# Kernel optimization log

Hardware: AMD Instinct MI355X
Metric: run time of the kernel (lower is better)

The kernel has to match this reference:

```python
import jax, jax.numpy as jnp
import numpy as np
import math

B, C, W, H = 4, 64, 128, 128
S = 2                 # len(shifts)
SHIFTS = (1, 2)       # dilations
HC = C // S           # hidden_channels = 32
NL = 8                # num_layer (8 diff stencils)
AREA = W * H
EPS = 1e-5


def _base_kernels():
    # 4 forward diff stencils + their 180-degree flips (delta2 = delta1[:, :, ::-1, ::-1])
    d1 = np.array([[[-1, 0, 0], [0, 1, 0], [0, 0, 0]],
                   [[0, -1, 0], [0, 1, 0], [0, 0, 0]],
                   [[0, 0, -1], [0, 1, 0], [0, 0, 0]],
                   [[0, 0, 0], [0, 1, -1], [0, 0, 0]]], dtype=np.float32).reshape(4, 1, 3, 3)
    d2 = d1[:, :, ::-1, ::-1].copy()
    return np.concatenate([d1, d2], axis=0)  # (8, 1, 3, 3)

# Depthwise kernel: per input channel, all 8 stencils (feature_group_count=HC layout)
_DW_KERNEL = jnp.asarray(np.tile(_base_kernels()[None], (HC, 1, 1, 1, 1)).reshape(NL * HC, 1, 3, 3))


def setup_inputs() -> dict:
    key = jax.random.key(0)
    ks = jax.random.split(key, 6)
    s = 0.05
    return {
        "x": jax.random.normal(ks[0], (B, C, W, H), jnp.float32),
        "trans_w": jax.random.normal(ks[1], (C, C), jnp.float32) * s,
        "bn1_g": jnp.ones((C,), jnp.float32),
        "bn1_b": jnp.zeros((C,), jnp.float32),
        "query_w": jax.random.normal(ks[2], (S, HC, HC), jnp.float32) * s,
        "key_w": jax.random.normal(ks[3], (S, (NL + 1) * HC, (NL + 1) * HC), jnp.float32) * s,
        "out_w": jax.random.normal(ks[4], (C, C), jnp.float32) * s,
        "bn2_g": jnp.ones((C,), jnp.float32),
        "bn2_b": jnp.zeros((C,), jnp.float32),
    }


def _bn_relu(y, g, b):
    # train-mode BatchNorm2d (biased batch stats) + ReLU
    m = y.mean((0, 2, 3), keepdims=True)
    v = y.var((0, 2, 3), keepdims=True)
    return jax.nn.relu((y - m) * jax.lax.rsqrt(v + EPS) * g[None, :, None, None] + b[None, :, None, None])


def _dw_diff_convs(x, dil):
    # x: (B, HC, W, H) -> 8 depthwise dilated 3x3 diff convs, concat order kernel-major
    y = jax.lax.conv_general_dilated(
        x, _DW_KERNEL, window_strides=(1, 1), padding='SAME',
        rhs_dilation=(dil, dil), feature_group_count=HC,
        dimension_numbers=('NCHW', 'OIHW', 'NCHW'))
    # grouped layout is (channel, stencil); torch concat order is (stencil, channel)
    return y.reshape(B, HC, NL, W, H).transpose(0, 2, 1, 3, 4).reshape(B, NL * HC, W, H)


def _inorm(w):
    # InstanceNorm2d(affine=False) over the last two dims, per (batch, shift)
    m = w.mean((-2, -1), keepdims=True)
    v = w.var((-2, -1), keepdims=True)
    return (w - m) * jax.lax.rsqrt(v + EPS)


def _l2n(x):
    # F.normalize(dim=-1)
    n = jnp.linalg.norm(x, axis=-1, keepdims=True)
    return x / jnp.maximum(n, 1e-12)


def reference(x, trans_w, bn1_g, bn1_b, query_w, key_w, out_w, bn2_g, bn2_b):
    y = _bn_relu(jnp.einsum('bchw,oc->bohw', x, trans_w), bn1_g, bn1_b)
    cens = y.reshape(B, S, HC, W, H)  # torch.chunk along channels
    keys, qrys, svs = [], [], []
    for i in range(S):
        c = cens[:, i]
        sur = _dw_diff_convs(c, SHIFTS[i])                                      # (B, 8*HC, W, H)
        kk = jnp.einsum('bchw,oc->bohw', jnp.concatenate([sur, c], 1), key_w[i])
        qq = jnp.einsum('bchw,oc->bohw', c, query_w[i])
        keys.append(kk.reshape(B, (NL + 1) * HC, AREA))
        qrys.append(qq.reshape(B, HC, AREA))
        svs.append(sur.reshape(B, NL * HC, AREA))
    keys = _l2n(jnp.stack(keys, 1))     # (B, S, 9*HC, AREA)
    qrys = _l2n(jnp.stack(qrys, 1))     # (B, S, HC, AREA)
    svs = jnp.stack(svs, 1)             # (B, S, 8*HC, AREA)
    w = jnp.einsum('bsca,bska->bsck', qrys, keys) / math.sqrt(AREA)  # (B, S, HC, 9*HC)
    sw = jax.nn.softmax(_inorm(w[..., :NL * HC]), axis=-1)           # (B, S, HC, 8*HC)
    out = jnp.einsum('bsck,bska->bsca', sw, svs).reshape(B, C, W, H)
    return _bn_relu(jnp.einsum('bchw,oc->bohw', out, out_w), bn2_g, bn2_b)
```

## Files before the change

kernel.cpp:

```cpp
#include <hip/hip_runtime.h>

#define BB 4
#define CC 64
#define SS 2
#define HCC 32
#define AREA_ 16384
#define KDIM 288
#define YPITCH 44

typedef _Float16 half8 __attribute__((ext_vector_type(8)));
typedef float f32x16 __attribute__((ext_vector_type(16)));

static __device__ __forceinline__ float warp_rsum(float v){
#pragma unroll
  for (int o=32;o>0;o>>=1) v += __shfl_down(v,o,64);
  return v;
}
static __device__ __forceinline__ float warp_rmax(float v){
#pragma unroll
  for (int o=32;o>0;o>>=1) v = fmaxf(v,__shfl_down(v,o,64));
  return v;
}

__global__ __launch_bounds__(256) void conv64_kernel(const float* __restrict__ in,
    const float* __restrict__ wmat, float* __restrict__ out){
  int b = blockIdx.x >> 7;
  int p0 = (blockIdx.x & 127) << 7;
  __shared__ float tile[64][132];
  __shared__ float wsm[64][68];
  for (int idx = threadIdx.x; idx < 4096; idx += 256){
    int c = idx & 63, o = idx >> 6;
    wsm[c][o] = wmat[o*64 + c];
  }
  const float* inb = in + (size_t)b*CC*AREA_ + p0;
  for (int idx = threadIdx.x; idx < 8192; idx += 256){
    int c = idx >> 7, pp = idx & 127;
    tile[c][pp] = inb[(size_t)c*AREA_ + pp];
  }
  __syncthreads();
  int px = (threadIdx.x & 31) * 4;
  int og = threadIdx.x >> 5;
  float4 acc[8];
#pragma unroll
  for (int i=0;i<8;i++) acc[i] = make_float4(0.f,0.f,0.f,0.f);
  for (int c=0;c<64;c++){
    float4 v  = *(const float4*)&tile[c][px];
    float4 w0 = *(const float4*)&wsm[c][og*8];
    float4 w1 = *(const float4*)&wsm[c][og*8+4];
    float wv[8] = {w0.x,w0.y,w0.z,w0.w,w1.x,w1.y,w1.z,w1.w};
#pragma unroll
    for (int i=0;i<8;i++){
      acc[i].x = fmaf(wv[i], v.x, acc[i].x);
      acc[i].y = fmaf(wv[i], v.y, acc[i].y);
      acc[i].z = fmaf(wv[i], v.z, acc[i].z);
      acc[i].w = fmaf(wv[i], v.w, acc[i].w);
    }
  }
  float* ob = out + (size_t)b*CC*AREA_ + p0 + px;
#pragma unroll
  for (int i=0;i<8;i++)
    *(float4*)&ob[(size_t)(og*8+i)*AREA_] = acc[i];
}

__global__ __launch_bounds__(256) void bn_part_kernel(const float* __restrict__ src,
    float* __restrict__ part){
  int c = blockIdx.x, chunk = blockIdx.y;
  float s1=0.f, s2=0.f;
  for (int b=0;b<BB;b++){
    const float* p = src + ((size_t)b*CC + c)*AREA_ + chunk*2048;
    for (int i=threadIdx.x;i<2048;i+=256){ float v=p[i]; s1+=v; s2+=v*v; }
  }
  __shared__ float red[8];
  float w1 = warp_rsum(s1), w2 = warp_rsum(s2);
  int lane = threadIdx.x & 63, wid = threadIdx.x >> 6;
  if (lane==0){ red[wid]=w1; red[4+wid]=w2; }
  __syncthreads();
  if (threadIdx.x==0){
    atomicAdd(&part[c], red[0]+red[1]+red[2]+red[3]);
    atomicAdd(&part[64+c], red[4]+red[5]+red[6]+red[7]);
  }
}

__global__ void bn_fin_kernel(const float* __restrict__ part, const float* __restrict__ gam,
    const float* __restrict__ bet, float* __restrict__ sb){
  int c = threadIdx.x;
  const float N = (float)(BB*AREA_);
  float m = part[c]/N;
  float var = part[64+c]/N - m*m;
  float sc = gam[c]*rsqrtf(var + 1e-5f);
  sb[c] = sc;
  sb[64+c] = bet[c] - m*sc;
}

__global__ __launch_bounds__(256) void bn_apply_relu_kernel(const float* __restrict__ src,
    const float* __restrict__ sb, float* __restrict__ dst){
  size_t i = (size_t)blockIdx.x*256 + threadIdx.x;
  int c = (int)((i >> 14) & 63);
  float v = fmaf(src[i], sb[c], sb[64+c]);
  dst[i] = v > 0.f ? v : 0.f;
}

__global__ __launch_bounds__(256) void qq_kernel(const float* __restrict__ y,
    const float* __restrict__ qw, float* __restrict__ qq){
  int blk = blockIdx.x;
  int p0 = (blk & 127) << 7;
  int s = (blk >> 7) & 1;
  int b = blk >> 8;
  __shared__ float tile[32][132];
  __shared__ float wsm[32][36];
  const float* qws = qw + s*HCC*HCC;
  for (int idx=threadIdx.x; idx<1024; idx+=256){
    int c = idx & 31, o = idx >> 5;
    wsm[c][o] = qws[o*32 + c];
  }
  const float* yb = y + ((size_t)b*CC + s*HCC)*AREA_ + p0;
  for (int idx=threadIdx.x; idx<4096; idx+=256){
    int c=idx>>7, pp=idx&127;
    tile[c][pp] = yb[(size_t)c*AREA_ + pp];
  }
  __syncthreads();
  int px = (threadIdx.x & 31) * 4;
  int og = threadIdx.x >> 5;
  float4 acc[4];
#pragma unroll
  for (int i=0;i<4;i++) acc[i] = make_float4(0.f,0.f,0.f,0.f);
  for (int c=0;c<32;c++){
    float4 v  = *(const float4*)&tile[c][px];
    float4 w0 = *(const float4*)&wsm[c][og*4];
    float wv[4] = {w0.x,w0.y,w0.z,w0.w};
#pragma unroll
    for (int i=0;i<4;i++){
      acc[i].x = fmaf(wv[i], v.x, acc[i].x);
      acc[i].y = fmaf(wv[i], v.y, acc[i].y);
      acc[i].z = fmaf(wv[i], v.z, acc[i].z);
      acc[i].w = fmaf(wv[i], v.w, acc[i].w);
    }
  }
  float* ob = qq + ((size_t)(b*SS+s)*HCC)*AREA_ + p0 + px;
#pragma unroll
  for (int i=0;i<4;i++)
    *(float4*)&ob[(size_t)(og*4+i)*AREA_] = acc[i];
}

__global__ __launch_bounds__(256,2) void gram_kernel(const float* __restrict__ y,
    const float* __restrict__ qq, float* __restrict__ dpart, float* __restrict__ wpart){
  const int PAarr[6]={0,0,1,0,1,2}, PBarr[6]={0,1,1,2,2,2};
  const int pairOrder[6]={1,3,4,0,2,5};
  const int pairbase[6]={0,262144,524288,786432,917504,1048576};
  const int tsz[6]={16384,16384,16384,8192,8192,4096};
  int bid = blockIdx.x;
  int bs = bid & 7;
  int sidx = bid >> 3;
  int pair = pairOrder[sidx >> 4];
  int slotIdx = sidx & 15;
  int Kstart = slotIdx << 10;
  const int nch = 16;
  int PA = PAarr[pair], PB = PBarr[pair];
  int RA = PA<2?128:64, CB = PB<2?128:64;
  bool diag = (PA==PB);
  int rows_tot = RA + (diag?0:CB);
  int passes = rows_tot >> 5;
  int s = bs & 1, b = bs >> 1, dil = 1+s;
  const float* yb = y + ((size_t)b*CC + s*HCC)*AREA_;
  const float* qqb = qq + (size_t)bs*HCC*AREA_;
  __shared__ __align__(16) _Float16 Us[256*64];
  int tid = threadIdx.x;
  int hq = tid & 7, rr8 = tid >> 3;
  int lane = tid & 63, wid = tid >> 6;
  int rbase = (wid>>1)*64, cbase = (wid&1)*64;
  bool active = (rbase < RA) && (cbase < CB);
  int boff = diag ? 0 : RA;
  int r0 = rbase + (lane&31), r1 = r0+32;
  int cr0 = boff + cbase + (lane&31), cr1 = cr0+32;
  int uo = lane>>5;

  auto loadPass = [&](int t, int p)->half8{
    int k0 = Kstart + t*64;
    int w = k0>>7, h = (k0&127) + hq*8;
    int pr = p*32 + rr8;
    int pan, prow;
    if (pr < RA){ pan = PA; prow = pr; } else { pan = PB; prow = pr - RA; }
    float vv[8];
    if (pan < 2){
      int l = pan*4 + (prow>>5), ch = prow & 31;
      int oy = ((0x6A40 >> (2*l)) & 3) - 1;
      int ox = ((0x6A4  >> (2*l)) & 3) - 1;
      const float* crow = yb + (size_t)ch*AREA_ + w*128 + h;
      float4 ca = *(const float4*)crow;
      float4 cb = *(const float4*)(crow+4);
      float cen[8] = {ca.x,ca.y,ca.z,ca.w,cb.x,cb.y,cb.z,cb.w};
      float nb[8];
      int wy = w + oy*dil, oxd = ox*dil, hb = h + oxd;
      if (wy>=0 && wy<128){
        const float* nrow = yb + (size_t)ch*AREA_ + wy*128 + hb;
        if (hb>=0 && hb<=120){
          float4 na, nc;
          __builtin_memcpy(&na, nrow, 16);
          __builtin_memcpy(&nc, nrow+4, 16);
          nb[0]=na.x; nb[1]=na.y; nb[2]=na.z; nb[3]=na.w;
          nb[4]=nc.x; nb[5]=nc.y; nb[6]=nc.z; nb[7]=nc.w;
        } else {
#pragma unroll
          for (int j=0;j<8;j++){
            int hx = hb + j;
            nb[j] = (hx>=0 && hx<128) ? nrow[j] : 0.f;
          }
        }
      } else {
#pragma unroll
        for (int j=0;j<8;j++) nb[j]=0.f;
      }
#pragma unroll
      for (int j=0;j<8;j++) vv[j] = cen[j]-nb[j];
    } else {
      const float* src = (prow<32) ? yb + (size_t)prow*AREA_ : qqb + (size_t)(prow-32)*AREA_;
      const float* crow = src + w*128 + h;
      float4 ca = *(const float4*)crow;
      float4 cb = *(const float4*)(crow+4);
      vv[0]=ca.x; vv[1]=ca.y; vv[2]=ca.z; vv[3]=ca.w;
      vv[4]=cb.x; vv[5]=cb.y; vv[6]=cb.z; vv[7]=cb.w;
    }
    half8 hv;
#pragma unroll
    for (int j=0;j<8;j++) hv[j] = (_Float16)vv[j];
    return hv;
  };
  auto writeLDS = [&](int p, half8 hv){
    int pr = p*32 + rr8;
    *(half8*)&Us[(size_t)pr*64 + ((hq ^ (pr&7))<<3)] = hv;
  };

  bool p4 = (passes >= 4), p6 = (passes >= 6), p8 = (passes >= 8);
  half8 f0{}, f1{}, f2{}, f3{}, f4{}, f5{}, f6{}, f7{};

  f32x16 acc00={}, acc01={}, acc10={}, acc11={};
  f0 = loadPass(0,0); f1 = loadPass(0,1);
  if (p4){ f2 = loadPass(0,2); f3 = loadPass(0,3); }
  if (p6){ f4 = loadPass(0,4); f5 = loadPass(0,5); }
  if (p8){ f6 = loadPass(0,6); f7 = loadPass(0,7); }
  for (int t=0; t<nch; ++t){
    asm volatile("s_waitcnt lgkmcnt(0)" ::: "memory");
    __builtin_amdgcn_s_barrier();
    writeLDS(0,f0); writeLDS(1,f1);
    if (p4){ writeLDS(2,f2); writeLDS(3,f3); }
    if (p6){ writeLDS(4,f4); writeLDS(5,f5); }
    if (p8){ writeLDS(6,f6); writeLDS(7,f7); }
    if (t+1 < nch){
      f0 = loadPass(t+1,0); f1 = loadPass(t+1,1);
      if (p4){ f2 = loadPass(t+1,2); f3 = loadPass(t+1,3); }
      if (p6){ f4 = loadPass(t+1,4); f5 = loadPass(t+1,5); }
      if (p8){ f6 = loadPass(t+1,6); f7 = loadPass(t+1,7); }
    }
    asm volatile("s_waitcnt lgkmcnt(0)" ::: "memory");
    __builtin_amdgcn_s_barrier();
    if (active){
#pragma unroll
      for (int st=0; st<4; ++st){
        int u = st*2 + uo;
        half8 a0 = *(const half8*)&Us[(size_t)r0*64  + ((u^(r0&7))<<3)];
        half8 a1 = *(const half8*)&Us[(size_t)r1*64  + ((u^(r1&7))<<3)];
        half8 b0 = *(const half8*)&Us[(size_t)cr0*64 + ((u^(cr0&7))<<3)];
        half8 b1 = *(const half8*)&Us[(size_t)cr1*64 + ((u^(cr1&7))<<3)];
        acc00 = __builtin_amdgcn_mfma_f32_32x32x16_f16(a0,b0,acc00,0,0,0);
        acc01 = __builtin_amdgcn_mfma_f32_32x32x16_f16(a0,b1,acc01,0,0,0);
        acc10 = __builtin_amdgcn_mfma_f32_32x32x16_f16(a1,b0,acc10,0,0,0);
        acc11 = __builtin_amdgcn_mfma_f32_32x32x16_f16(a1,b1,acc11,0,0,0);
      }
    }
  }
  if (active){
    size_t off = (size_t)bs*1114112 + pairbase[pair] + (size_t)slotIdx*tsz[pair];
    float* pp = (off < 4194304) ? (dpart + off) : (wpart + (off - 4194304));
    int cp = (pair<3)?128:64;
    int rr = 4*uo, cc = lane&31;
#pragma unroll
    for (int reg=0;reg<16;reg++){
      int ro = (reg&3) + 8*(reg>>2) + rr;
      pp[(size_t)(rbase+ro)*cp + cbase+cc]       = acc00[reg];
      pp[(size_t)(rbase+ro)*cp + cbase+32+cc]    = acc01[reg];
      pp[(size_t)(rbase+32+ro)*cp + cbase+cc]    = acc10[reg];
      pp[(size_t)(rbase+32+ro)*cp + cbase+32+cc] = acc11[reg];
    }
  }
}

__global__ __launch_bounds__(256) void reduce_kernel(const float* __restrict__ dpart,
    const float* __restrict__ wpart, float* __restrict__ P){
  const int PAarr[6]={0,0,1,0,1,2}, PBarr[6]={0,1,1,2,2,2};
  const int pairbase[6]={0,262144,524288,786432,917504,1048576};
  const int tsz[6]={16384,16384,16384,8192,8192,4096};
  const int chunkbase[7]={0,16,32,48,56,64,68};
  int chunk = blockIdx.x, bs = blockIdx.y;
  int pair = 0;
  while (chunk >= chunkbase[pair+1]) pair++;
  int lc = chunk - chunkbase[pair];
  int CN = (pair<3)?128:64;
  int Roff = PAarr[pair]*128, Coff = PBarr[pair]*128;
  int csh = (CN==128)?7:6;
  int cell0 = lc*1024 + threadIdx.x*4;
  int r = cell0 >> csh, c = cell0 & (CN-1);
  float4 v = make_float4(0.f,0.f,0.f,0.f);
  size_t base = (size_t)bs*1114112 + pairbase[pair];
  for (int k=0;k<16;k++){
    size_t off = base + (size_t)k*tsz[pair];
    const float* pp = (off < 4194304) ? (dpart + off) : (wpart + (off - 4194304));
    float4 t = *(const float4*)&pp[(size_t)r*CN + c];
    v.x += t.x; v.y += t.y; v.z += t.z; v.w += t.w;
  }
  float* Pb = P + (size_t)bs*102400;
  *(float4*)&Pb[(size_t)(Roff+r)*320 + Coff+c] = v;
  Pb[(size_t)(Coff+c  )*320 + Roff+r] = v.x;
  Pb[(size_t)(Coff+c+1)*320 + Roff+r] = v.y;
  Pb[(size_t)(Coff+c+2)*320 + Roff+r] = v.z;
  Pb[(size_t)(Coff+c+3)*320 + Roff+r] = v.w;
}

__global__ __launch_bounds__(256) void kwT_kernel(const float* __restrict__ kw, float* __restrict__ kwT){
  int idx = blockIdx.x*256 + threadIdx.x;
  if (idx >= 2*KDIM*KDIM) return;
  int s = idx / (KDIM*KDIM);
  int r = idx - s*KDIM*KDIM;
  int k = r / KDIM, j = r - k*KDIM;
  kwT[(size_t)s*KDIM*KDIM + (size_t)j*KDIM + k] = kw[idx];
}

__global__ __launch_bounds__(256) void vknorm_kernel(const float* __restrict__ P,
    const float* __restrict__ kwT, float* __restrict__ kn){
  int j = blockIdx.x, bs = blockIdx.y;
  int s = bs & 1;
  __shared__ float prow[KDIM];
  const float* Pb = P + (size_t)bs*102400 + (size_t)j*320;
  for (int i=threadIdx.x;i<KDIM;i+=256) prow[i]=Pb[i];
  __syncthreads();
  const float* kt = kwT + (size_t)s*KDIM*KDIM;
  int k = threadIdx.x;
  float acc=0.f;
  for (int jp=0;jp<KDIM;jp++) acc = fmaf(prow[jp], kt[(size_t)jp*KDIM + k], acc);
  atomicAdd(&kn[bs*256 + k], kt[(size_t)j*KDIM + k] * acc);
}

__global__ __launch_bounds__(256) void wmat_kernel(const float* __restrict__ P,
    const float* __restrict__ kwT, const float* __restrict__ kn,
    float* __restrict__ wbuf, float* __restrict__ wstats){
  int bs = blockIdx.x >> 5, c = blockIdx.x & 31;
  int s = bs & 1;
  __shared__ float prow[KDIM];
  const float* PbB = P + (size_t)bs*102400;
  const float* Pb = PbB + (size_t)(288+c)*320;
  for (int i=threadIdx.x;i<KDIM;i+=256) prow[i]=Pb[i];
  __syncthreads();
  const float* kt = kwT + (size_t)s*KDIM*KDIM;
  int k = threadIdx.x;
  float acc=0.f;
  for (int j=0;j<KDIM;j++) acc = fmaf(prow[j], kt[(size_t)j*KDIM + k], acc);
  float rk = 1.f/fmaxf(sqrtf(fmaxf(kn[bs*256+k],0.f)),1e-12f);
  float qn = PbB[(size_t)(288+c)*320 + 288+c];
  float rq = 1.f/fmaxf(sqrtf(fmaxf(qn,0.f)),1e-12f);
  float wv = acc * rq * rk * (1.f/128.f);
  wbuf[((size_t)bs*32 + c)*256 + k] = wv;
  __shared__ float red[8];
  float r1 = warp_rsum(wv), r2 = warp_rsum(wv*wv);
  int lane = threadIdx.x & 63, wid = threadIdx.x >> 6;
  if (lane==0){ red[wid]=r1; red[4+wid]=r2; }
  __syncthreads();
  if (threadIdx.x==0){
    atomicAdd(&wstats[bs*2],   red[0]+red[1]+red[2]+red[3]);
    atomicAdd(&wstats[bs*2+1], red[4]+red[5]+red[6]+red[7]);
  }
}

__global__ __launch_bounds__(256) void smx_kernel(const float* __restrict__ wbuf,
    const float* __restrict__ wstats, float* __restrict__ sw){
  int bs = blockIdx.x >> 5, c = blockIdx.x & 31;
  float s1 = wstats[bs*2], s2 = wstats[bs*2+1];
  const float N = 8192.f;
  float m = s1/N, var = s2/N - m*m;
  float rs = rsqrtf(var + 1e-5f);
  int k = threadIdx.x;
  float v = (wbuf[((size_t)bs*32 + c)*256 + k] - m)*rs;
  __shared__ float red[4];
  float mx = warp_rmax(v);
  int lane = k & 63, wid = k >> 6;
  if (lane==0) red[wid]=mx;
  __syncthreads();
  float MX = fmaxf(fmaxf(red[0],red[1]),fmaxf(red[2],red[3]));
  __syncthreads();
  float e = expf(v - MX);
  float es = warp_rsum(e);
  if (lane==0) red[wid]=es;
  __syncthreads();
  float ES = red[0]+red[1]+red[2]+red[3];
  sw[((size_t)bs*32 + c)*256 + k] = e/ES;
}

__global__ __launch_bounds__(256) void tswf_kernel(const float* __restrict__ sw, _Float16* __restrict__ tswf){
  int idx = blockIdx.x*256 + threadIdx.x;
  if (idx >= 9216) return;
  int lane = idx & 63;
  int ks = (idx >> 6) % 18;
  int bs = idx / (18*64);
  int c = lane & 31;
  const float* swb = sw + ((size_t)bs*32 + c)*256;
  half8 hv;
#pragma unroll
  for (int j=0;j<8;j++){
    int k = ks*16 + ((lane>>5)<<3) + j;
    int t = k >> 5, ch = k & 31;
    float v;
    if (t==0){ v=0.f; for (int l=0;l<8;l++) v += swb[l*32+ch]; }
    else v = -swb[(t-1)*32 + ch];
    hv[j] = (_Float16)v;
  }
  *(half8*)&tswf[(size_t)idx*8] = hv;
}

__global__ __launch_bounds__(256,2) void attn_mfma_kernel(const float* __restrict__ y,
    const _Float16* __restrict__ tswf, float* __restrict__ outs){
  int blk = blockIdx.x;
  int w = blk & 127;
  int s = (blk >> 7) & 1;
  int b = blk >> 8;
  int bs = b*SS + s;
  int dil = 1 + s;
  __shared__ __align__(16) _Float16 ybuf[3*132*YPITCH];
  const float* yb = y + ((size_t)bs*HCC)*AREA_;
  int tid = threadIdx.x;
  int lane = tid & 63, wid = tid >> 6;

  const _Float16* tf = tswf + ((size_t)bs*18*64 + lane)*8;
  half8 afr[18];
#pragma unroll
  for (int ks=0; ks<18; ++ks) afr[ks] = *(const half8*)&tf[(size_t)ks*64*8];

  for (int i = tid; i < 384; i += 256){
    int ch = i & 31;
    int q = i >> 5;
    int wr = q >> 2, hb = q & 3;
    int hi = (hb < 2) ? hb : (128 + hb);
    int oct = (ch>>3) ^ ((hi>>2)&3);
    ybuf[(size_t)(wr*132+hi)*YPITCH + oct*8 + (ch&7)] = (_Float16)0.f;
  }
  int ch8 = tid >> 5;
  int h4 = (tid & 31) * 4;
#pragma unroll
  for (int r = 0; r < 12; ++r){
    int wr = r >> 2, chg = r & 3;
    int wy = w + (wr-1)*dil;
    if (wy < 0 || wy >= 128) continue;
    int ch = chg*8 + ch8;
    float4 v = *(const float4*)&yb[(size_t)ch*AREA_ + wy*128 + h4];
    float vv[4] = {v.x, v.y, v.z, v.w};
#pragma unroll
    for (int j=0;j<4;j++){
      int hi = h4 + 2 + j;
      int oct = (ch>>3) ^ ((hi>>2)&3);
      ybuf[(size_t)(wr*132+hi)*YPITCH + oct*8 + (ch&7)] = (_Float16)vv[j];
    }
  }
  __syncthreads();

  const int offy[9]={0,-1,-1,-1,0,1,1,1,0};
  const int offx[9]={0,-1,0,1,1,1,0,-1,-1};
  int n0 = wid * 32;
  int nl = n0 + (lane & 31);
  int ko = lane >> 5;
  f32x16 acc = {};
#pragma unroll
  for (int ks=0; ks<18; ++ks){
    int t = ks >> 1;
    int wy = w + offy[t]*dil;
    half8 bfr = {};
    if (wy >= 0 && wy < 128){
      int wr = offy[t] + 1;
      int hi = nl + offx[t]*dil + 2;
      int oct = (((ks&1)<<1) | ko) ^ ((hi>>2)&3);
      bfr = *(const half8*)&ybuf[(size_t)(wr*132+hi)*YPITCH + oct*8];
    }
    acc = __builtin_amdgcn_mfma_f32_32x32x16_f16(afr[ks], bfr, acc, 0,0,0);
  }
  float* ob = outs + (size_t)bs*HCC*AREA_ + (size_t)w*128;
  int col = n0 + (lane & 31);
  int rb = 4*(lane>>5);
#pragma unroll
  for (int reg=0; reg<16; ++reg){
    int c = (reg&3) + 8*(reg>>2) + rb;
    ob[(size_t)c*AREA_ + col] = acc[reg];
  }
}

extern "C" void kernel_launch(void* const* d_in, const int* in_sizes, int n_in,
                              void* d_out, int out_size, void* d_ws, size_t ws_size,
                              hipStream_t stream){
  const float* x   = (const float*)d_in[0];
  const float* tw  = (const float*)d_in[1];
  const float* g1  = (const float*)d_in[2];
  const float* b1  = (const float*)d_in[3];
  const float* qw  = (const float*)d_in[4];
  const float* kw  = (const float*)d_in[5];
  const float* ow  = (const float*)d_in[6];
  const float* g2  = (const float*)d_in[7];
  const float* b2  = (const float*)d_in[8];
  float* out = (float*)d_out;
  float* ws = (float*)d_ws;

  float* y      = ws + 64;
  float* qqb    = ws + 4194368;
  float* kwT    = qqb;
  float* wbuf   = ws + 4360256;
  float* wpart  = ws + 8388672;
  float* outs   = wpart;
  float* P      = ws + 13107264;
  float* stats  = ws + 13926464;
  float* wstats = ws + 13926720;
  float* kn     = ws + 13926976;
  float* sb     = ws + 13929024;
  float* swb    = ws + 13929280;
  _Float16* tswf = (_Float16*)(ws + 13994816);
  float* dpart  = (float*)d_out;
  float* z      = y;

  hipMemsetAsync(stats, 0, 2560*sizeof(float), stream);

  conv64_kernel<<<512,256,0,stream>>>(x, tw, y);
  bn_part_kernel<<<dim3(64,8),256,0,stream>>>(y, stats);
  bn_fin_kernel<<<1,64,0,stream>>>(stats, g1, b1, sb);
  bn_apply_relu_kernel<<<16384,256,0,stream>>>(y, sb, y);
  qq_kernel<<<1024,256,0,stream>>>(y, qw, qqb);
  gram_kernel<<<768,256,0,stream>>>(y, qqb, dpart, wpart);
  reduce_kernel<<<dim3(68,8),256,0,stream>>>(dpart, wpart, P);
  kwT_kernel<<<648,256,0,stream>>>(kw, kwT);
  vknorm_kernel<<<dim3(288,8),256,0,stream>>>(P, kwT, kn);
  wmat_kernel<<<256,256,0,stream>>>(P, kwT, kn, wbuf, wstats);
  smx_kernel<<<256,256,0,stream>>>(wbuf, wstats, swb);
  tswf_kernel<<<36,256,0,stream>>>(swb, tswf);
  attn_mfma_kernel<<<1024,256,0,stream>>>(y, tswf, outs);
  conv64_kernel<<<512,256,0,stream>>>(outs, ow, z);
  bn_part_kernel<<<dim3(64,8),256,0,stream>>>(z, stats+128);
  bn_fin_kernel<<<1,64,0,stream>>>(stats+128, g2, b2, sb+128);
  bn_apply_relu_kernel<<<16384,256,0,stream>>>(z, sb+128, out);
}
```

Baseline: 259.8 us.

## Fuse BN finalize into apply kernel and widen gram kernel to 512 threads

Removes the separate single-block BN finalize kernel by computing per-channel scale and bias inside the BN apply kernel, so two tiny launches and their serialization points go away. The Gram MFMA kernel moves from 256 to 512 threads per block. Each wave now computes a 64x32 output tile instead of 64x64, and each thread loads half as many staging passes. This halves per-thread registers and accumulators and raises the wave count for latency hiding, at the cost of more redundant A-fragment LDS reads. The BN apply kernel now recomputes the statistics per element, which costs a few extra loads and an rsqrt per thread.

```diff
diff --git a/kernel.cpp b/kernel.cpp
--- a/kernel.cpp
+++ b/kernel.cpp
@@ -81,22 +81,17 @@
   }
 }
 
-__global__ void bn_fin_kernel(const float* __restrict__ part, const float* __restrict__ gam,
-    const float* __restrict__ bet, float* __restrict__ sb){
-  int c = threadIdx.x;
+__global__ __launch_bounds__(256) void bn_apply_relu_kernel(const float* __restrict__ src,
+    const float* __restrict__ part, const float* __restrict__ gam,
+    const float* __restrict__ bet, float* __restrict__ dst){
+  size_t i = (size_t)blockIdx.x*256 + threadIdx.x;
+  int c = (int)((i >> 14) & 63);
   const float N = (float)(BB*AREA_);
   float m = part[c]/N;
   float var = part[64+c]/N - m*m;
   float sc = gam[c]*rsqrtf(var + 1e-5f);
-  sb[c] = sc;
-  sb[64+c] = bet[c] - m*sc;
-}
-
-__global__ __launch_bounds__(256) void bn_apply_relu_kernel(const float* __restrict__ src,
-    const float* __restrict__ sb, float* __restrict__ dst){
-  size_t i = (size_t)blockIdx.x*256 + threadIdx.x;
-  int c = (int)((i >> 14) & 63);
-  float v = fmaf(src[i], sb[c], sb[64+c]);
+  float bi = bet[c] - m*sc;
+  float v = fmaf(src[i], sc, bi);
   dst[i] = v > 0.f ? v : 0.f;
 }
 
@@ -142,7 +137,7 @@
     *(float4*)&ob[(size_t)(og*4+i)*AREA_] = acc[i];
 }
 
-__global__ __launch_bounds__(256,2) void gram_kernel(const float* __restrict__ y,
+__global__ __launch_bounds__(512) void gram_kernel(const float* __restrict__ y,
     const float* __restrict__ qq, float* __restrict__ dpart, float* __restrict__ wpart){
   const int PAarr[6]={0,0,1,0,1,2}, PBarr[6]={0,1,1,2,2,2};
   const int pairOrder[6]={1,3,4,0,2,5};
@@ -159,7 +154,7 @@
   int RA = PA<2?128:64, CB = PB<2?128:64;
   bool diag = (PA==PB);
   int rows_tot = RA + (diag?0:CB);
-  int passes = rows_tot >> 5;
+  int passes = rows_tot >> 6;
   int s = bs & 1, b = bs >> 1, dil = 1+s;
   const float* yb = y + ((size_t)b*CC + s*HCC)*AREA_;
   const float* qqb = qq + (size_t)bs*HCC*AREA_;
@@ -167,17 +162,17 @@
   int tid = threadIdx.x;
   int hq = tid & 7, rr8 = tid >> 3;
   int lane = tid & 63, wid = tid >> 6;
-  int rbase = (wid>>1)*64, cbase = (wid&1)*64;
+  int rbase = (wid>>2)*64, cbase = (wid&3)*32;
   bool active = (rbase < RA) && (cbase < CB);
   int boff = diag ? 0 : RA;
   int r0 = rbase + (lane&31), r1 = r0+32;
-  int cr0 = boff + cbase + (lane&31), cr1 = cr0+32;
+  int cr = boff + cbase + (lane&31);
   int uo = lane>>5;
 
   auto loadPass = [&](int t, int p)->half8{
     int k0 = Kstart + t*64;
     int w = k0>>7, h = (k0&127) + hq*8;
-    int pr = p*32 + rr8;
+    int pr = p*64 + rr8;
     int pan, prow;
     if (pr < RA){ pan = PA; prow = pr; } else { pan = PB; prow = pr - RA; }
     float vv[8];
@@ -226,30 +221,30 @@
     return hv;
   };
   auto writeLDS = [&](int p, half8 hv){
-    int pr = p*32 + rr8;
+    int pr = p*64 + rr8;
     *(half8*)&Us[(size_t)pr*64 + ((hq ^ (pr&7))<<3)] = hv;
   };
 
-  bool p4 = (passes >= 4), p6 = (passes >= 6), p8 = (passes >= 8);
-  half8 f0{}, f1{}, f2{}, f3{}, f4{}, f5{}, f6{}, f7{};
-
-  f32x16 acc00={}, acc01={}, acc10={}, acc11={};
-  f0 = loadPass(0,0); f1 = loadPass(0,1);
-  if (p4){ f2 = loadPass(0,2); f3 = loadPass(0,3); }
-  if (p6){ f4 = loadPass(0,4); f5 = loadPass(0,5); }
-  if (p8){ f6 = loadPass(0,6); f7 = loadPass(0,7); }
+  bool p2 = (passes >= 2), p3 = (passes >= 3), p4 = (passes >= 4);
+  half8 f0{}, f1{}, f2{}, f3{};
+
+  f32x16 acc0={}, acc1={};
+  f0 = loadPass(0,0);
+  if (p2) f1 = loadPass(0,1);
+  if (p3) f2 = loadPass(0,2);
+  if (p4) f3 = loadPass(0,3);
   for (int t=0; t<nch; ++t){
     asm volatile("s_waitcnt lgkmcnt(0)" ::: "memory");
     __builtin_amdgcn_s_barrier();
-    writeLDS(0,f0); writeLDS(1,f1);
-    if (p4){ writeLDS(2,f2); writeLDS(3,f3); }
-    if (p6){ writeLDS(4,f4); writeLDS(5,f5); }
-    if (p8){ writeLDS(6,f6); writeLDS(7,f7); }
+    writeLDS(0,f0);
+    if (p2) writeLDS(1,f1);
+    if (p3) writeLDS(2,f2);
+    if (p4) writeLDS(3,f3);
     if (t+1 < nch){
-      f0 = loadPass(t+1,0); f1 = loadPass(t+1,1);
-      if (p4){ f2 = loadPass(t+1,2); f3 = loadPass(t+1,3); }
-      if (p6){ f4 = loadPass(t+1,4); f5 = loadPass(t+1,5); }
-      if (p8){ f6 = loadPass(t+1,6); f7 = loadPass(t+1,7); }
+      f0 = loadPass(t+1,0);
+      if (p2) f1 = loadPass(t+1,1);
+      if (p3) f2 = loadPass(t+1,2);
+      if (p4) f3 = loadPass(t+1,3);
     }
     asm volatile("s_waitcnt lgkmcnt(0)" ::: "memory");
     __builtin_amdgcn_s_barrier();
@@ -257,14 +252,11 @@
 #pragma unroll
       for (int st=0; st<4; ++st){
         int u = st*2 + uo;
-        half8 a0 = *(const half8*)&Us[(size_t)r0*64  + ((u^(r0&7))<<3)];
-        half8 a1 = *(const half8*)&Us[(size_t)r1*64  + ((u^(r1&7))<<3)];
-        half8 b0 = *(const half8*)&Us[(size_t)cr0*64 + ((u^(cr0&7))<<3)];
-        half8 b1 = *(const half8*)&Us[(size_t)cr1*64 + ((u^(cr1&7))<<3)];
-        acc00 = __builtin_amdgcn_mfma_f32_32x32x16_f16(a0,b0,acc00,0,0,0);
-        acc01 = __builtin_amdgcn_mfma_f32_32x32x16_f16(a0,b1,acc01,0,0,0);
-        acc10 = __builtin_amdgcn_mfma_f32_32x32x16_f16(a1,b0,acc10,0,0,0);
-        acc11 = __builtin_amdgcn_mfma_f32_32x32x16_f16(a1,b1,acc11,0,0,0);
+        half8 a0 = *(const half8*)&Us[(size_t)r0*64 + ((u^(r0&7))<<3)];
+        half8 a1 = *(const half8*)&Us[(size_t)r1*64 + ((u^(r1&7))<<3)];
+        half8 bb = *(const half8*)&Us[(size_t)cr*64 + ((u^(cr&7))<<3)];
+        acc0 = __builtin_amdgcn_mfma_f32_32x32x16_f16(a0,bb,acc0,0,0,0);
+        acc1 = __builtin_amdgcn_mfma_f32_32x32x16_f16(a1,bb,acc1,0,0,0);
       }
     }
   }
@@ -276,10 +268,8 @@
 #pragma unroll
     for (int reg=0;reg<16;reg++){
       int ro = (reg&3) + 8*(reg>>2) + rr;
-      pp[(size_t)(rbase+ro)*cp + cbase+cc]       = acc00[reg];
-      pp[(size_t)(rbase+ro)*cp + cbase+32+cc]    = acc01[reg];
-      pp[(size_t)(rbase+32+ro)*cp + cbase+cc]    = acc10[reg];
-      pp[(size_t)(rbase+32+ro)*cp + cbase+32+cc] = acc11[reg];
+      pp[(size_t)(rbase+ro)*cp + cbase+cc]    = acc0[reg];
+      pp[(size_t)(rbase+32+ro)*cp + cbase+cc] = acc1[reg];
     }
   }
 }
@@ -513,7 +503,6 @@
   float* stats  = ws + 13926464;
   float* wstats = ws + 13926720;
   float* kn     = ws + 13926976;
-  float* sb     = ws + 13929024;
   float* swb    = ws + 13929280;
   _Float16* tswf = (_Float16*)(ws + 13994816);
   float* dpart  = (float*)d_out;
@@ -523,10 +512,9 @@
 
   conv64_kernel<<<512,256,0,stream>>>(x, tw, y);
   bn_part_kernel<<<dim3(64,8),256,0,stream>>>(y, stats);
-  bn_fin_kernel<<<1,64,0,stream>>>(stats, g1, b1, sb);
-  bn_apply_relu_kernel<<<16384,256,0,stream>>>(y, sb, y);
+  bn_apply_relu_kernel<<<16384,256,0,stream>>>(y, stats, g1, b1, y);
   qq_kernel<<<1024,256,0,stream>>>(y, qw, qqb);
-  gram_kernel<<<768,256,0,stream>>>(y, qqb, dpart, wpart);
+  gram_kernel<<<768,512,0,stream>>>(y, qqb, dpart, wpart);
   reduce_kernel<<<dim3(68,8),256,0,stream>>>(dpart, wpart, P);
   kwT_kernel<<<648,256,0,stream>>>(kw, kwT);
   vknorm_kernel<<<dim3(288,8),256,0,stream>>>(P, kwT, kn);
@@ -536,6 +524,5 @@
   attn_mfma_kernel<<<1024,256,0,stream>>>(y, tswf, outs);
   conv64_kernel<<<512,256,0,stream>>>(outs, ow, z);
   bn_part_kernel<<<dim3(64,8),256,0,stream>>>(z, stats+128);
-  bn_fin_kernel<<<1,64,0,stream>>>(stats+128, g2, b2, sb+128);
-  bn_apply_relu_kernel<<<16384,256,0,stream>>>(z, sb+128, out);
-}
+  bn_apply_relu_kernel<<<16384,256,0,stream>>>(z, stats+128, g2, b2, out);
+}
```

Measured after the change: 249.8 us. 3.9% less time.
